# Performance work log

Hardware: AMD Instinct MI355X
Metric: run time of the kernel (lower is better)

The kernel has to match this reference:

```python
import jax, jax.numpy as jnp
import numpy as np

B, H, V, T = 2048, 512, 64, 128

def setup_inputs() -> dict:
    key = jax.random.key(0)
    ks = jax.random.split(key, 7)
    s = 1.0 / np.sqrt(H)
    return {
        "z": jax.random.normal(ks[0], (B, H), dtype=jnp.float32),
        "w_ih": jax.random.uniform(ks[1], (4 * H, H), jnp.float32, -s, s),
        "w_hh": jax.random.uniform(ks[2], (4 * H, H), jnp.float32, -s, s),
        "b_ih": jax.random.uniform(ks[3], (4 * H,), jnp.float32, -s, s),
        "b_hh": jax.random.uniform(ks[4], (4 * H,), jnp.float32, -s, s),
        "fc_w": jax.random.uniform(ks[5], (V, H), jnp.float32, -s, s),
        "fc_b": jax.random.uniform(ks[6], (V,), jnp.float32, -s, s),
    }

def reference(z, w_ih, w_hh, b_ih, b_hh, fc_w, fc_b):
    batch = z.shape[0]
    # Input z is identical at every timestep -> precompute its gate contribution once.
    x_gates = z @ w_ih.T + b_ih + b_hh  # [B, 4H]

    def step(carry, _):
        h, c = carry
        gates = x_gates + h @ w_hh.T  # [B, 4H]
        i, f, g, o = jnp.split(gates, 4, axis=-1)  # PyTorch LSTMCell gate order
        i = jax.nn.sigmoid(i)
        f = jax.nn.sigmoid(f)
        g = jnp.tanh(g)
        o = jax.nn.sigmoid(o)
        c = f * c + i * g
        h = o * jnp.tanh(c)
        return (h, c), h

    h0 = jnp.zeros((batch, w_hh.shape[1]), dtype=z.dtype)
    c0 = jnp.zeros_like(h0)
    _, hs = jax.lax.scan(step, (h0, c0), None, length=T)  # [T, B, H]
    x = jnp.transpose(hs, (1, 0, 2))  # [B, T, H]
    return jax.nn.relu(x @ fc_w.T + fc_b)  # [B, T, V]
```

## Files before the change

kernel.cpp:

```cpp
#include <hip/hip_runtime.h>
#include <hip/hip_bf16.h>
#include <cstdint>

#define B_   2048
#define H_   512
#define T_   128
#define V_   64
#define FOURH 2048

typedef __bf16 bf16x8 __attribute__((ext_vector_type(8)));
typedef float  floatx4 __attribute__((ext_vector_type(4)));
typedef int    intx4   __attribute__((ext_vector_type(4)));

__device__ __forceinline__ unsigned short f2bf(float f) {
    union { float f; uint32_t u; } v; v.f = f;
    uint32_t r = v.u + 0x7fff + ((v.u >> 16) & 1);
    return (unsigned short)(r >> 16);
}

__device__ __forceinline__ float rcp_(float x) {
    float r; asm("v_rcp_f32 %0, %1" : "=v"(r) : "v"(x)); return r;
}
__device__ __forceinline__ float sigmoidf_(float x) {
    return rcp_(1.0f + __expf(-x));
}
__device__ __forceinline__ float tanhf_(float x) {
    float e = __expf(fminf(-2.0f * x, 80.0f));
    return (1.0f - e) * rcp_(1.0f + e);
}

__device__ __forceinline__ void global_to_lds16(const unsigned short* g, unsigned short* l) {
    __builtin_amdgcn_global_load_lds(
        (const __attribute__((address_space(1))) unsigned int*)g,
        (__attribute__((address_space(3))) unsigned int*)l, 16, 0, 0);
}

__device__ __forceinline__ bf16x8 load16_sys(const unsigned short* p) {
    bf16x8 d;
    asm volatile("global_load_dwordx4 %0, %1, off sc0 sc1\n\t"
                 "s_waitcnt vmcnt(0)"
                 : "=v"(d) : "v"(p));
    return d;
}

__device__ __forceinline__ void flag_prefetch(const unsigned int* fp, intx4& f) {
    asm volatile("global_load_dwordx4 %0, %1, off sc0 sc1"
                 : "=v"(f) : "v"(fp) : "memory");
}
__device__ __forceinline__ bool flag_ok(const intx4& f, unsigned int tgt) {
    return (unsigned int)f[0] >= tgt && (unsigned int)f[1] >= tgt &&
           (unsigned int)f[2] >= tgt && (unsigned int)f[3] >= tgt;
}
__device__ __forceinline__ void wait4(const unsigned int* fp, unsigned int tgt) {
    for (;;) {
        intx4 f;
        asm volatile("global_load_dwordx4 %0, %1, off sc0 sc1\n\t"
                     "s_waitcnt vmcnt(0)" : "=v"(f) : "v"(fp) : "memory");
        if (flag_ok(f, tgt)) return;
        __builtin_amdgcn_s_sleep(1);
    }
}
__device__ __forceinline__ void flag_post(unsigned int* p, unsigned int v) {
    asm volatile("global_store_dword %0, %1, off sc0 sc1" :: "v"(p), "v"(v) : "memory");
}

__global__ void prep_kernel(const float* __restrict__ z,
                            const float* __restrict__ w_ih,
                            const float* __restrict__ w_hh,
                            const float* __restrict__ b_ih,
                            const float* __restrict__ b_hh,
                            const float* __restrict__ fc_w,
                            unsigned short* __restrict__ Bp_ih,
                            unsigned short* __restrict__ Bp_hh,
                            unsigned short* __restrict__ z_bf,
                            unsigned short* __restrict__ fcw_bf,
                            float* __restrict__ biasp,
                            unsigned int* __restrict__ cnt) {
    int i = blockIdx.x * blockDim.x + threadIdx.x;
    int col = i >> 9, k = i & 511;
    int jj = col >> 7, cc = col & 127;
    int gate = (cc >> 4) & 3;
    int hcl = ((cc >> 6) << 4) | (cc & 15);
    int p = gate * 512 + jj * 32 + hcl;
    Bp_hh[i] = f2bf(w_hh[p * 512 + k]);
    Bp_ih[i] = f2bf(w_ih[p * 512 + k]);
    z_bf[i]  = f2bf(z[i]);
    if (i < V_ * H_) fcw_bf[i] = f2bf(fc_w[i]);
    if (i < FOURH) {
        int j2 = i >> 7, c2 = i & 127;
        int g2 = (c2 >> 4) & 3;
        int h2 = ((c2 >> 6) << 4) | (c2 & 15);
        int p2 = g2 * 512 + j2 * 32 + h2;
        biasp[i] = b_ih[p2] + b_hh[p2];
    }
    if (i < 2048) cnt[i] = 0;
}

__device__ __forceinline__ void gemm_tile_r1(
        const unsigned short* __restrict__ Aglob,
        const unsigned short* __restrict__ Bglob,
        int arow0, int brow0,
        unsigned short* As, unsigned short* Bs,
        floatx4 acc[2][8], int w, int l) {
    const int lr = l >> 3;
    const int gl = (l & 7) ^ lr;
    const int ln = l & 15, lq = l >> 4, ls = l & 7;
    for (int kc = 0; kc < 8; ++kc) {
        const int kof = kc * 64 + gl * 8;
        #pragma unroll
        for (int q = 0; q < 4; ++q) {
            const int r0 = (w * 4 + q) * 8;
            global_to_lds16(Aglob + (size_t)(arow0 + r0 + lr) * 512 + kof, As + r0 * 64);
            global_to_lds16(Bglob + (size_t)(brow0 + r0 + lr) * 512 + kof, Bs + r0 * 64);
        }
        __syncthreads();
        #pragma unroll
        for (int kk = 0; kk < 2; ++kk) {
            bf16x8 a[2], b[8];
            #pragma unroll
            for (int mt = 0; mt < 2; ++mt) {
                const int m = 32 * w + 16 * mt + ln;
                const int g = kk * 4 + lq;
                a[mt] = *(const bf16x8*)(As + m * 64 + ((g ^ ls) * 8));
            }
            #pragma unroll
            for (int nt = 0; nt < 8; ++nt) {
                const int n = 16 * nt + ln;
                const int g = kk * 4 + lq;
                b[nt] = *(const bf16x8*)(Bs + n * 64 + ((g ^ ls) * 8));
            }
            #pragma unroll
            for (int mt = 0; mt < 2; ++mt)
                #pragma unroll
                for (int nt = 0; nt < 8; ++nt)
                    acc[mt][nt] = __builtin_amdgcn_mfma_f32_16x16x32_bf16(
                        a[mt], b[nt], acc[mt][nt], 0, 0, 0);
        }
        __syncthreads();
    }
}

__global__ void __launch_bounds__(256) xg_gemm_kernel(
        const unsigned short* __restrict__ z_bf,
        const unsigned short* __restrict__ Bp_ih,
        const float* __restrict__ biasp,
        float* __restrict__ xg) {
    __shared__ unsigned short As[128 * 64];
    __shared__ unsigned short Bs[128 * 64];
    const int bi = blockIdx.x, j = blockIdx.y;
    const int tid = threadIdx.x, w = tid >> 6, l = tid & 63;
    floatx4 acc[2][8];
    const floatx4 zf = {0.f, 0.f, 0.f, 0.f};
    for (int a1 = 0; a1 < 2; ++a1) for (int a2 = 0; a2 < 8; ++a2) acc[a1][a2] = zf;

    gemm_tile_r1(z_bf, Bp_ih, bi * 128, j * 128, As, Bs, acc, w, l);

    const int ln = l & 15, lq = l >> 4;
    #pragma unroll
    for (int mt = 0; mt < 2; ++mt)
        #pragma unroll
        for (int nt = 0; nt < 8; ++nt) {
            const int colp = j * 128 + nt * 16 + ln;
            const float bv = biasp[colp];
            #pragma unroll
            for (int r = 0; r < 4; ++r) {
                const int b = bi * 128 + 32 * w + 16 * mt + lq * 4 + r;
                xg[(size_t)b * FOURH + colp] = acc[mt][nt][r] + bv;
            }
        }
}

__device__ __forceinline__ void stage_issue2(const unsigned short* __restrict__ Aglob,
                                             int arow0, int kc, int w, int l,
                                             intx4& t0, intx4& t1) {
    const int lr = l >> 3;
    const int gl = (l & 7) ^ lr;
    const int kof = kc * 64 + gl * 8;
    const unsigned short* p0 = Aglob + (size_t)(arow0 + (w * 2 + 0) * 8 + lr) * 512 + kof;
    const unsigned short* p1 = Aglob + (size_t)(arow0 + (w * 2 + 1) * 8 + lr) * 512 + kof;
    asm volatile(
        "global_load_dwordx4 %0, %2, off sc0 sc1\n\t"
        "global_load_dwordx4 %1, %3, off sc0 sc1"
        : "=&v"(t0), "=&v"(t1)
        : "v"(p0), "v"(p1)
        : "memory");
}

template<int N>
__device__ __forceinline__ void commit4c(unsigned short* buf, int w, int l,
                                         const intx4* u) {
    if constexpr (N == 12) asm volatile("s_waitcnt vmcnt(12)" ::: "memory");
    else if constexpr (N == 8)  asm volatile("s_waitcnt vmcnt(8)"  ::: "memory");
    else if constexpr (N == 4)  asm volatile("s_waitcnt vmcnt(4)"  ::: "memory");
    else                        asm volatile("s_waitcnt vmcnt(0)"  ::: "memory");
    const int lr = l >> 3, sl = (l & 7) * 8;
    #pragma unroll
    for (int kcL = 0; kcL < 2; ++kcL)
        #pragma unroll
        for (int q = 0; q < 2; ++q)
            *(intx4*)(buf + kcL * 4096 + ((w * 2 + q) * 8 + lr) * 64 + sl) = u[kcL * 2 + q];
}

__global__ void __launch_bounds__(256, 1) lstm_persistent(
        const unsigned short* __restrict__ Bp_hh,
        const unsigned short* __restrict__ fcw_bf,
        const float* __restrict__ xg,
        const float* __restrict__ fc_b,
        unsigned short* __restrict__ h0b,
        unsigned short* __restrict__ h1b,
        unsigned int* __restrict__ cnt,
        float* __restrict__ out) {
    __shared__ unsigned short AsB0[4096 * 2];
    __shared__ unsigned short AsB1[4096 * 2];

    const int bx = blockIdx.x;
    const int gi = bx & 31;
    const int j  = bx >> 5;
    const int tid = threadIdx.x;
    const int w = tid >> 6, l = tid & 63;
    const int ln = l & 15, lq = l >> 4;
    const bool jlt4 = (j < 4);
    const int j16 = j * 16;
    const int v = 16 * w + ln;
    const float fcb_v = fc_b[v];
    const int arow0 = gi * 64;
    const int colbase = j * 256 + (w >> 1) * 128 + (w & 1) * 64;
    unsigned int* flagp = cnt + gi * 64;
    const floatx4 zf = {0.f, 0.f, 0.f, 0.f};

    bf16x8 bq[16][4];
    {
        const unsigned short* bbase =
            Bp_hh + ((size_t)(colbase + ln)) * 512 + lq * 8;
        #pragma unroll
        for (int s = 0; s < 16; ++s)
            #pragma unroll
            for (int nt = 0; nt < 4; ++nt)
                bq[s][nt] = *(const bf16x8*)(bbase + (size_t)nt * 16 * 512 + s * 32);
    }

    floatx4 xga[4][4];
    #pragma unroll
    for (int mt = 0; mt < 4; ++mt)
        #pragma unroll
        for (int nt = 0; nt < 4; ++nt)
            #pragma unroll
            for (int r = 0; r < 4; ++r) {
                const int b = arow0 + 16 * mt + lq * 4 + r;
                xga[mt][nt][r] = xg[(size_t)b * FOURH + colbase + 16 * nt + ln];
            }

    for (int d = 0; d < gi; ++d) __builtin_amdgcn_s_sleep(15);

    unsigned short* hlds = AsB0;

    float cst[4][4];
    #pragma unroll
    for (int mt = 0; mt < 4; ++mt)
        #pragma unroll
        for (int r = 0; r < 4; ++r) {
            float iv = sigmoidf_(xga[mt][0][r]);
            float gv = tanhf_  (xga[mt][2][r]);
            float ov = sigmoidf_(xga[mt][3][r]);
            float cv = iv * gv;
            cst[mt][r] = cv;
            hlds[(16 * mt + lq * 4 + r) * 64 + (16 * w + ln)] = f2bf(ov * tanhf_(cv));
        }
    __syncthreads();
    for (int c = tid; c < 512; c += 256) {
        const int row = c >> 3, seg = c & 7;
        intx4 d = *(const intx4*)(hlds + row * 64 + seg * 8);
        const unsigned short* p = h0b + (size_t)(arow0 + row) * 512 + j * 64 + seg * 8;
        asm volatile("global_store_dwordx4 %0, %1, off sc0 sc1" :: "v"(p), "v"(d) : "memory");
    }
    asm volatile("s_waitcnt vmcnt(0)" ::: "memory");
    __syncthreads();
    if (tid == 0) flag_post(flagp + j, 1u);
    intx4 fpreA, fpreB;
    flag_prefetch(flagp,     fpreA);
    flag_prefetch(flagp + 4, fpreB);

    unsigned short* hb[2] = {h0b, h1b};
    #pragma unroll 1
    for (int t = 1; t < T_; ++t) {
        const unsigned int tg = (unsigned int)t;

        asm volatile("s_waitcnt vmcnt(0)" ::: "memory");
        __builtin_amdgcn_sched_barrier(0);
        if (!(flag_ok(fpreA, tg) && flag_ok(fpreB, tg))) {
            wait4(flagp, tg);
            wait4(flagp + 4, tg);
        }

        const unsigned short* hprev = hb[(t - 1) & 1];
        unsigned short* hnext = hb[t & 1];

        floatx4 acc[4][4];
        #pragma unroll
        for (int a1 = 0; a1 < 4; ++a1)
            #pragma unroll
            for (int a2 = 0; a2 < 4; ++a2) acc[a1][a2] = zf;
        floatx4 pacc = zf;

        intx4 u[16];
        #pragma unroll
        for (int g = 0; g < 4; ++g) {
            stage_issue2(hprev, arow0, 2 * g,     w, l, u[4 * g + 0], u[4 * g + 1]);
            stage_issue2(hprev, arow0, 2 * g + 1, w, l, u[4 * g + 2], u[4 * g + 3]);
        }
        commit4c<12>(AsB0, w, l, &u[0]);
        __syncthreads();

        #pragma unroll
        for (int g = 0; g < 4; ++g) {
            const unsigned short* buf = (g & 1) ? AsB1 : AsB0;
            #pragma unroll
            for (int ss = 0; ss < 4; ++ss) {
                const int s = g * 4 + ss;
                const int ga = (ss & 1) * 4 + lq;
                const unsigned short* Ac = buf + (ss >> 1) * 4096;
                bf16x8 af[4];
                #pragma unroll
                for (int mt = 0; mt < 4; ++mt) {
                    const int m = 16 * mt + ln;
                    af[mt] = *(const bf16x8*)(Ac + m * 64 + ((ga ^ (ln & 7)) * 8));
                }
                #pragma unroll
                for (int mt = 0; mt < 4; ++mt)
                    #pragma unroll
                    for (int nt = 0; nt < 4; ++nt)
                        acc[mt][nt] = __builtin_amdgcn_mfma_f32_16x16x32_bf16(
                            af[mt], bq[s][nt], acc[mt][nt], 0, 0, 0);
                if (jlt4) {
                    bf16x8 ap = *(const bf16x8*)(Ac + (j16 + ln) * 64 + ((ga ^ (ln & 7)) * 8));
                    bf16x8 bp = *(const bf16x8*)(fcw_bf + (size_t)v * 512 + s * 32 + lq * 8);
                    pacc = __builtin_amdgcn_mfma_f32_16x16x32_bf16(ap, bp, pacc, 0, 0, 0);
                }
            }
            if (g == 0) { commit4c<8>(AsB1, w, l, &u[4]);  __syncthreads(); }
            else if (g == 1) { commit4c<4>(AsB0, w, l, &u[8]);  __syncthreads(); }
            else if (g == 2) { commit4c<0>(AsB1, w, l, &u[12]); __syncthreads(); }
        }

        #pragma unroll
        for (int mt = 0; mt < 4; ++mt)
            #pragma unroll
            for (int r = 0; r < 4; ++r) {
                float iv = sigmoidf_(acc[mt][0][r] + xga[mt][0][r]);
                float fv = sigmoidf_(acc[mt][1][r] + xga[mt][1][r]);
                float gv = tanhf_  (acc[mt][2][r] + xga[mt][2][r]);
                float ov = sigmoidf_(acc[mt][3][r] + xga[mt][3][r]);
                float cn = fv * cst[mt][r] + iv * gv;
                cst[mt][r] = cn;
                hlds[(16 * mt + lq * 4 + r) * 64 + (16 * w + ln)] = f2bf(ov * tanhf_(cn));
            }
        __syncthreads();
        for (int c = tid; c < 512; c += 256) {
            const int row = c >> 3, seg = c & 7;
            intx4 d = *(const intx4*)(hlds + row * 64 + seg * 8);
            const unsigned short* p = hnext + (size_t)(arow0 + row) * 512 + j * 64 + seg * 8;
            asm volatile("global_store_dwordx4 %0, %1, off sc0 sc1" :: "v"(p), "v"(d) : "memory");
        }
        asm volatile("s_waitcnt vmcnt(0)" ::: "memory");
        __syncthreads();
        if (tid == 0) flag_post(flagp + j, tg + 1u);

        if (jlt4) {
            #pragma unroll
            for (int r = 0; r < 4; ++r) {
                const int b = arow0 + j16 + lq * 4 + r;
                out[(size_t)b * (T_ * V_) + (t - 1) * V_ + v] = fmaxf(pacc[r] + fcb_v, 0.0f);
            }
        }
        flag_prefetch(flagp,     fpreA);
        flag_prefetch(flagp + 4, fpreB);
    }

    if (jlt4) {
        wait4(flagp,     T_);
        wait4(flagp + 4, T_);
        const unsigned short* hlast = hb[(T_ - 1) & 1];
        floatx4 pa = zf;
        const int ar = arow0 + j16 + ln;
        #pragma unroll
        for (int kc = 0; kc < 16; ++kc) {
            const int k = kc * 32 + lq * 8;
            bf16x8 a = load16_sys(hlast + (size_t)ar * 512 + k);
            bf16x8 b = *(const bf16x8*)(fcw_bf + (size_t)v * 512 + k);
            pa = __builtin_amdgcn_mfma_f32_16x16x32_bf16(a, b, pa, 0, 0, 0);
        }
        #pragma unroll
        for (int r = 0; r < 4; ++r) {
            const int b = arow0 + j16 + lq * 4 + r;
            out[(size_t)b * (T_ * V_) + (T_ - 1) * V_ + v] = fmaxf(pa[r] + fcb_v, 0.0f);
        }
    }
}

extern "C" void kernel_launch(void* const* d_in, const int* in_sizes, int n_in,
                              void* d_out, int out_size, void* d_ws, size_t ws_size,
                              hipStream_t stream) {
    const float* z    = (const float*)d_in[0];
    const float* w_ih = (const float*)d_in[1];
    const float* w_hh = (const float*)d_in[2];
    const float* b_ih = (const float*)d_in[3];
    const float* b_hh = (const float*)d_in[4];
    const float* fc_w = (const float*)d_in[5];
    const float* fc_b = (const float*)d_in[6];
    float* out = (float*)d_out;

    char* ws = (char*)d_ws;
    size_t o = 0;
    auto take = [&](size_t bytes) { char* p = ws + o; o += (bytes + 255) & ~(size_t)255; return p; };
    unsigned short* Bp_hh  = (unsigned short*)take((size_t)FOURH * H_ * 2);
    unsigned short* Bp_ih  = (unsigned short*)take((size_t)FOURH * H_ * 2);
    unsigned short* z_bf   = (unsigned short*)take((size_t)B_ * H_ * 2);
    unsigned short* fcw_bf = (unsigned short*)take((size_t)V_ * H_ * 2);
    float*          biasp  = (float*)take((size_t)FOURH * 4);
    unsigned short* hbuf0  = (unsigned short*)take((size_t)B_ * H_ * 2);
    unsigned short* hbuf1  = (unsigned short*)take((size_t)B_ * H_ * 2);
    unsigned int*   cnt    = (unsigned int*)take(32 * 256);
    float*          xg     = (float*)take((size_t)B_ * FOURH * 4);

    prep_kernel<<<(B_ * H_) / 256, 256, 0, stream>>>(z, w_ih, w_hh, b_ih, b_hh, fc_w,
                                                     Bp_ih, Bp_hh, z_bf, fcw_bf, biasp, cnt);
    xg_gemm_kernel<<<dim3(16, 16), 256, 0, stream>>>(z_bf, Bp_ih, biasp, xg);
    lstm_persistent<<<256, 256, 0, stream>>>(Bp_hh, fcw_bf, xg, fc_b,
                                             hbuf0, hbuf1, cnt, out);
}
```

Before: 1.483 ms.

## Split batch tile into two half-phases to overlap h exchange with compute

```diff
diff --git a/kernel.cpp b/kernel.cpp
--- a/kernel.cpp
+++ b/kernel.cpp
@@ -170,35 +170,123 @@
         }
 }
 
-__device__ __forceinline__ void stage_issue2(const unsigned short* __restrict__ Aglob,
-                                             int arow0, int kc, int w, int l,
-                                             intx4& t0, intx4& t1) {
-    const int lr = l >> 3;
-    const int gl = (l & 7) ^ lr;
-    const int kof = kc * 64 + gl * 8;
-    const unsigned short* p0 = Aglob + (size_t)(arow0 + (w * 2 + 0) * 8 + lr) * 512 + kof;
-    const unsigned short* p1 = Aglob + (size_t)(arow0 + (w * 2 + 1) * 8 + lr) * 512 + kof;
-    asm volatile(
-        "global_load_dwordx4 %0, %2, off sc0 sc1\n\t"
-        "global_load_dwordx4 %1, %3, off sc0 sc1"
-        : "=&v"(t0), "=&v"(t1)
-        : "v"(p0), "v"(p1)
-        : "memory");
-}
-
-template<int N>
-__device__ __forceinline__ void commit4c(unsigned short* buf, int w, int l,
-                                         const intx4* u) {
-    if constexpr (N == 12) asm volatile("s_waitcnt vmcnt(12)" ::: "memory");
-    else if constexpr (N == 8)  asm volatile("s_waitcnt vmcnt(8)"  ::: "memory");
-    else if constexpr (N == 4)  asm volatile("s_waitcnt vmcnt(4)"  ::: "memory");
-    else                        asm volatile("s_waitcnt vmcnt(0)"  ::: "memory");
-    const int lr = l >> 3, sl = (l & 7) * 8;
-    #pragma unroll
-    for (int kcL = 0; kcL < 2; ++kcL)
-        #pragma unroll
-        for (int q = 0; q < 2; ++q)
-            *(intx4*)(buf + kcL * 4096 + ((w * 2 + q) * 8 + lr) * 64 + sl) = u[kcL * 2 + q];
+template<int HF>
+__device__ __forceinline__ void phase_body(
+        int t, bool last,
+        int arow0, int j, int tid, int w, int l, int ln, int lq,
+        bool my_half, int j16, int v, float fcb_v,
+        unsigned short* hb0, unsigned short* hb1,
+        unsigned int* flagp,
+        unsigned short* Xlds, unsigned short* hlds,
+        const unsigned short* __restrict__ fcw_bf,
+        const bf16x8 (&bq)[16][4],
+        floatx4 (&acc)[2][4], float (&cst)[2][4], const floatx4 (&xga)[2][4],
+        floatx4& pacc, float* __restrict__ out,
+        intx4 (&u)[8], intx4& fp0, intx4& fp1)
+{
+    const unsigned int V = (unsigned int)t + (unsigned int)HF;
+    const int foff = 8 * (1 - HF);
+    unsigned short* hbt[2] = {hb0, hb1};
+    const floatx4 zf = {0.f, 0.f, 0.f, 0.f};
+
+    asm volatile("s_waitcnt vmcnt(0)" ::: "memory");
+    __builtin_amdgcn_sched_barrier(0);
+
+    if (tid == 0) flag_post(flagp + foff + j, V);
+    {
+        const int lr = l >> 3, sl = (l & 7) * 8;
+        #pragma unroll
+        for (int kc = 0; kc < 8; ++kc)
+            *(intx4*)(Xlds + kc * 2048 + (w * 8 + lr) * 64 + sl) = u[kc];
+    }
+    __syncthreads();
+
+    if (!last) {
+        flag_prefetch(flagp + foff,     fp0);
+        flag_prefetch(flagp + foff + 4, fp1);
+    }
+    if (my_half) pacc = zf;
+    #pragma unroll
+    for (int s = 0; s < 16; ++s) {
+        const int ga = (s & 1) * 4 + lq;
+        const unsigned short* Ac = Xlds + (s >> 1) * 2048;
+        bf16x8 af[2];
+        #pragma unroll
+        for (int mt = 0; mt < 2; ++mt)
+            af[mt] = *(const bf16x8*)(Ac + (16 * mt + ln) * 64 + ((ga ^ (ln & 7)) * 8));
+        #pragma unroll
+        for (int mt = 0; mt < 2; ++mt)
+            #pragma unroll
+            for (int nt = 0; nt < 4; ++nt)
+                acc[mt][nt] = __builtin_amdgcn_mfma_f32_16x16x32_bf16(
+                    af[mt], bq[s][nt], acc[mt][nt], 0, 0, 0);
+        if (my_half) {
+            bf16x8 ap = *(const bf16x8*)(Ac + ((j16 & 31) + ln) * 64 + ((ga ^ (ln & 7)) * 8));
+            bf16x8 bp = *(const bf16x8*)(fcw_bf + (size_t)v * 512 + s * 32 + lq * 8);
+            pacc = __builtin_amdgcn_mfma_f32_16x16x32_bf16(ap, bp, pacc, 0, 0, 0);
+        }
+    }
+
+    if (!last) {
+        asm volatile("s_waitcnt vmcnt(0)" ::: "memory");
+        __builtin_amdgcn_sched_barrier(0);
+        if (!(flag_ok(fp0, V) && flag_ok(fp1, V))) {
+            wait4(flagp + foff,     V);
+            wait4(flagp + foff + 4, V);
+        }
+        if (my_half) {
+            #pragma unroll
+            for (int r = 0; r < 4; ++r) {
+                const int b = arow0 + j16 + lq * 4 + r;
+                out[(size_t)b * (T_ * V_) + (t - 1) * V_ + v] = fmaxf(pacc[r] + fcb_v, 0.0f);
+            }
+        }
+        {
+            const unsigned short* src = hbt[(t - 1 + HF) & 1]
+                                      + (size_t)(arow0 + (1 - HF) * 32) * 512;
+            const int lr = l >> 3;
+            const int gl = (l & 7) ^ lr;
+            #pragma unroll
+            for (int kc = 0; kc < 8; ++kc) {
+                const unsigned short* p = src + (size_t)(w * 8 + lr) * 512 + kc * 64 + gl * 8;
+                asm volatile("global_load_dwordx4 %0, %1, off sc0 sc1"
+                             : "=&v"(u[kc]) : "v"(p) : "memory");
+            }
+        }
+    } else {
+        if (my_half) {
+            #pragma unroll
+            for (int r = 0; r < 4; ++r) {
+                const int b = arow0 + j16 + lq * 4 + r;
+                out[(size_t)b * (T_ * V_) + (t - 1) * V_ + v] = fmaxf(pacc[r] + fcb_v, 0.0f);
+            }
+        }
+    }
+
+    #pragma unroll
+    for (int mt = 0; mt < 2; ++mt)
+        #pragma unroll
+        for (int r = 0; r < 4; ++r) {
+            float iv = sigmoidf_(acc[mt][0][r] + xga[mt][0][r]);
+            float fv = sigmoidf_(acc[mt][1][r] + xga[mt][1][r]);
+            float gv = tanhf_  (acc[mt][2][r] + xga[mt][2][r]);
+            float ov = sigmoidf_(acc[mt][3][r] + xga[mt][3][r]);
+            float cn = fv * cst[mt][r] + iv * gv;
+            cst[mt][r] = cn;
+            hlds[(16 * mt + lq * 4 + r) * 64 + (16 * w + ln)] = f2bf(ov * tanhf_(cn));
+        }
+    #pragma unroll
+    for (int mt = 0; mt < 2; ++mt)
+        #pragma unroll
+        for (int nt = 0; nt < 4; ++nt) acc[mt][nt] = zf;
+    __syncthreads();
+    {
+        const int row = tid >> 3, seg = tid & 7;
+        intx4 d = *(const intx4*)(hlds + row * 64 + seg * 8);
+        const unsigned short* p = hbt[t & 1]
+                                + (size_t)(arow0 + HF * 32 + row) * 512 + j * 64 + seg * 8;
+        asm volatile("global_store_dwordx4 %0, %1, off sc0 sc1" :: "v"(p), "v"(d) : "memory");
+    }
 }
 
 __global__ void __launch_bounds__(256, 1) lstm_persistent(
@@ -210,8 +298,9 @@
         unsigned short* __restrict__ h1b,
         unsigned int* __restrict__ cnt,
         float* __restrict__ out) {
-    __shared__ unsigned short AsB0[4096 * 2];
-    __shared__ unsigned short AsB1[4096 * 2];
+    __shared__ unsigned short Alds[8 * 2048];
+    __shared__ unsigned short Blds[8 * 2048];
+    __shared__ unsigned short hlds[2048];
 
     const int bx = blockIdx.x;
     const int gi = bx & 31;
@@ -227,6 +316,8 @@
     const int colbase = j * 256 + (w >> 1) * 128 + (w & 1) * 64;
     unsigned int* flagp = cnt + gi * 64;
     const floatx4 zf = {0.f, 0.f, 0.f, 0.f};
+    const bool myA = jlt4 && (j < 2);
+    const bool myB = jlt4 && (j >= 2);
 
     bf16x8 bq[16][4];
     {
@@ -239,147 +330,105 @@
                 bq[s][nt] = *(const bf16x8*)(bbase + (size_t)nt * 16 * 512 + s * 32);
     }
 
-    floatx4 xga[4][4];
-    #pragma unroll
-    for (int mt = 0; mt < 4; ++mt)
+    floatx4 xgaA[2][4], xgaB[2][4];
+    #pragma unroll
+    for (int mt = 0; mt < 2; ++mt)
         #pragma unroll
         for (int nt = 0; nt < 4; ++nt)
             #pragma unroll
             for (int r = 0; r < 4; ++r) {
-                const int b = arow0 + 16 * mt + lq * 4 + r;
-                xga[mt][nt][r] = xg[(size_t)b * FOURH + colbase + 16 * nt + ln];
+                const int ba = arow0 + 16 * mt + lq * 4 + r;
+                const int bb = arow0 + 32 + 16 * mt + lq * 4 + r;
+                xgaA[mt][nt][r] = xg[(size_t)ba * FOURH + colbase + 16 * nt + ln];
+                xgaB[mt][nt][r] = xg[(size_t)bb * FOURH + colbase + 16 * nt + ln];
             }
 
     for (int d = 0; d < gi; ++d) __builtin_amdgcn_s_sleep(15);
 
-    unsigned short* hlds = AsB0;
-
-    float cst[4][4];
-    #pragma unroll
-    for (int mt = 0; mt < 4; ++mt)
+    float cstA[2][4], cstB[2][4];
+    floatx4 accA[2][4], accB[2][4];
+    #pragma unroll
+    for (int mt = 0; mt < 2; ++mt)
+        #pragma unroll
+        for (int nt = 0; nt < 4; ++nt) { accA[mt][nt] = zf; accB[mt][nt] = zf; }
+
+    #pragma unroll
+    for (int mt = 0; mt < 2; ++mt)
         #pragma unroll
         for (int r = 0; r < 4; ++r) {
-            float iv = sigmoidf_(xga[mt][0][r]);
-            float gv = tanhf_  (xga[mt][2][r]);
-            float ov = sigmoidf_(xga[mt][3][r]);
+            float iv = sigmoidf_(xgaA[mt][0][r]);
+            float gv = tanhf_  (xgaA[mt][2][r]);
+            float ov = sigmoidf_(xgaA[mt][3][r]);
             float cv = iv * gv;
-            cst[mt][r] = cv;
+            cstA[mt][r] = cv;
             hlds[(16 * mt + lq * 4 + r) * 64 + (16 * w + ln)] = f2bf(ov * tanhf_(cv));
         }
     __syncthreads();
-    for (int c = tid; c < 512; c += 256) {
-        const int row = c >> 3, seg = c & 7;
+    {
+        const int row = tid >> 3, seg = tid & 7;
         intx4 d = *(const intx4*)(hlds + row * 64 + seg * 8);
         const unsigned short* p = h0b + (size_t)(arow0 + row) * 512 + j * 64 + seg * 8;
         asm volatile("global_store_dwordx4 %0, %1, off sc0 sc1" :: "v"(p), "v"(d) : "memory");
     }
+    __syncthreads();
+    #pragma unroll
+    for (int mt = 0; mt < 2; ++mt)
+        #pragma unroll
+        for (int r = 0; r < 4; ++r) {
+            float iv = sigmoidf_(xgaB[mt][0][r]);
+            float gv = tanhf_  (xgaB[mt][2][r]);
+            float ov = sigmoidf_(xgaB[mt][3][r]);
+            float cv = iv * gv;
+            cstB[mt][r] = cv;
+            hlds[(16 * mt + lq * 4 + r) * 64 + (16 * w + ln)] = f2bf(ov * tanhf_(cv));
+        }
+    __syncthreads();
+    {
+        const int row = tid >> 3, seg = tid & 7;
+        intx4 d = *(const intx4*)(hlds + row * 64 + seg * 8);
+        const unsigned short* p = h0b + (size_t)(arow0 + 32 + row) * 512 + j * 64 + seg * 8;
+        asm volatile("global_store_dwordx4 %0, %1, off sc0 sc1" :: "v"(p), "v"(d) : "memory");
+    }
     asm volatile("s_waitcnt vmcnt(0)" ::: "memory");
     __syncthreads();
-    if (tid == 0) flag_post(flagp + j, 1u);
-    intx4 fpreA, fpreB;
-    flag_prefetch(flagp,     fpreA);
-    flag_prefetch(flagp + 4, fpreB);
-
-    unsigned short* hb[2] = {h0b, h1b};
+    if (tid == 0) { flag_post(flagp + j, 1u); flag_post(flagp + 8 + j, 1u); }
+
+    wait4(flagp,     1u);
+    wait4(flagp + 4, 1u);
+    intx4 u[8];
+    {
+        const unsigned short* src = h0b + (size_t)arow0 * 512;
+        const int lr = l >> 3;
+        const int gl = (l & 7) ^ lr;
+        #pragma unroll
+        for (int kc = 0; kc < 8; ++kc) {
+            const unsigned short* p = src + (size_t)(w * 8 + lr) * 512 + kc * 64 + gl * 8;
+            asm volatile("global_load_dwordx4 %0, %1, off sc0 sc1"
+                         : "=&v"(u[kc]) : "v"(p) : "memory");
+        }
+    }
+
+    floatx4 pacc = zf;
+    intx4 fp0, fp1;
     #pragma unroll 1
     for (int t = 1; t < T_; ++t) {
-        const unsigned int tg = (unsigned int)t;
-
-        asm volatile("s_waitcnt vmcnt(0)" ::: "memory");
-        __builtin_amdgcn_sched_barrier(0);
-        if (!(flag_ok(fpreA, tg) && flag_ok(fpreB, tg))) {
-            wait4(flagp, tg);
-            wait4(flagp + 4, tg);
-        }
-
-        const unsigned short* hprev = hb[(t - 1) & 1];
-        unsigned short* hnext = hb[t & 1];
-
-        floatx4 acc[4][4];
-        #pragma unroll
-        for (int a1 = 0; a1 < 4; ++a1)
-            #pragma unroll
-            for (int a2 = 0; a2 < 4; ++a2) acc[a1][a2] = zf;
-        floatx4 pacc = zf;
-
-        intx4 u[16];
-        #pragma unroll
-        for (int g = 0; g < 4; ++g) {
-            stage_issue2(hprev, arow0, 2 * g,     w, l, u[4 * g + 0], u[4 * g + 1]);
-            stage_issue2(hprev, arow0, 2 * g + 1, w, l, u[4 * g + 2], u[4 * g + 3]);
-        }
-        commit4c<12>(AsB0, w, l, &u[0]);
-        __syncthreads();
-
-        #pragma unroll
-        for (int g = 0; g < 4; ++g) {
-            const unsigned short* buf = (g & 1) ? AsB1 : AsB0;
-            #pragma unroll
-            for (int ss = 0; ss < 4; ++ss) {
-                const int s = g * 4 + ss;
-                const int ga = (ss & 1) * 4 + lq;
-                const unsigned short* Ac = buf + (ss >> 1) * 4096;
-                bf16x8 af[4];
-                #pragma unroll
-                for (int mt = 0; mt < 4; ++mt) {
-                    const int m = 16 * mt + ln;
-                    af[mt] = *(const bf16x8*)(Ac + m * 64 + ((ga ^ (ln & 7)) * 8));
-                }
-                #pragma unroll
-                for (int mt = 0; mt < 4; ++mt)
-                    #pragma unroll
-                    for (int nt = 0; nt < 4; ++nt)
-                        acc[mt][nt] = __builtin_amdgcn_mfma_f32_16x16x32_bf16(
-                            af[mt], bq[s][nt], acc[mt][nt], 0, 0, 0);
-                if (jlt4) {
-                    bf16x8 ap = *(const bf16x8*)(Ac + (j16 + ln) * 64 + ((ga ^ (ln & 7)) * 8));
-                    bf16x8 bp = *(const bf16x8*)(fcw_bf + (size_t)v * 512 + s * 32 + lq * 8);
-                    pacc = __builtin_amdgcn_mfma_f32_16x16x32_bf16(ap, bp, pacc, 0, 0, 0);
-                }
-            }
-            if (g == 0) { commit4c<8>(AsB1, w, l, &u[4]);  __syncthreads(); }
-            else if (g == 1) { commit4c<4>(AsB0, w, l, &u[8]);  __syncthreads(); }
-            else if (g == 2) { commit4c<0>(AsB1, w, l, &u[12]); __syncthreads(); }
-        }
-
-        #pragma unroll
-        for (int mt = 0; mt < 4; ++mt)
-            #pragma unroll
-            for (int r = 0; r < 4; ++r) {
-                float iv = sigmoidf_(acc[mt][0][r] + xga[mt][0][r]);
-                float fv = sigmoidf_(acc[mt][1][r] + xga[mt][1][r]);
-                float gv = tanhf_  (acc[mt][2][r] + xga[mt][2][r]);
-                float ov = sigmoidf_(acc[mt][3][r] + xga[mt][3][r]);
-                float cn = fv * cst[mt][r] + iv * gv;
-                cst[mt][r] = cn;
-                hlds[(16 * mt + lq * 4 + r) * 64 + (16 * w + ln)] = f2bf(ov * tanhf_(cn));
-            }
-        __syncthreads();
-        for (int c = tid; c < 512; c += 256) {
-            const int row = c >> 3, seg = c & 7;
-            intx4 d = *(const intx4*)(hlds + row * 64 + seg * 8);
-            const unsigned short* p = hnext + (size_t)(arow0 + row) * 512 + j * 64 + seg * 8;
-            asm volatile("global_store_dwordx4 %0, %1, off sc0 sc1" :: "v"(p), "v"(d) : "memory");
-        }
-        asm volatile("s_waitcnt vmcnt(0)" ::: "memory");
-        __syncthreads();
-        if (tid == 0) flag_post(flagp + j, tg + 1u);
-
-        if (jlt4) {
-            #pragma unroll
-            for (int r = 0; r < 4; ++r) {
-                const int b = arow0 + j16 + lq * 4 + r;
-                out[(size_t)b * (T_ * V_) + (t - 1) * V_ + v] = fmaxf(pacc[r] + fcb_v, 0.0f);
-            }
-        }
-        flag_prefetch(flagp,     fpreA);
-        flag_prefetch(flagp + 4, fpreB);
-    }
+        phase_body<0>(t, false, arow0, j, tid, w, l, ln, lq, myA, j16, v, fcb_v,
+                      h0b, h1b, flagp, Alds, hlds, fcw_bf, bq,
+                      accA, cstA, xgaA, pacc, out, u, fp0, fp1);
+        phase_body<1>(t, t == T_ - 1, arow0, j, tid, w, l, ln, lq, myB, j16, v, fcb_v,
+                      h0b, h1b, flagp, Blds, hlds, fcw_bf, bq,
+                      accB, cstB, xgaB, pacc, out, u, fp0, fp1);
+    }
+
+    asm volatile("s_waitcnt vmcnt(0)" ::: "memory");
+    __syncthreads();
+    if (tid == 0) flag_post(flagp + 8 + j, (unsigned int)T_);
 
     if (jlt4) {
-        wait4(flagp,     T_);
-        wait4(flagp + 4, T_);
-        const unsigned short* hlast = hb[(T_ - 1) & 1];
+        const int hf = (j >= 2);
+        wait4(flagp + 8 * hf,     (unsigned int)T_);
+        wait4(flagp + 8 * hf + 4, (unsigned int)T_);
+        const unsigned short* hlast = h1b;
         floatx4 pa = zf;
         const int ar = arow0 + j16 + ln;
         #pragma unroll
```

Result: faster. 1.417 ms (-4.4%).

## Split batch group into four 16-row slices with per-slice flags for pipelined recurrence

Applied to the files above, without the earlier changes.

```diff
diff --git a/kernel.cpp b/kernel.cpp
--- a/kernel.cpp
+++ b/kernel.cpp
@@ -170,35 +170,113 @@
         }
 }
 
-__device__ __forceinline__ void stage_issue2(const unsigned short* __restrict__ Aglob,
-                                             int arow0, int kc, int w, int l,
-                                             intx4& t0, intx4& t1) {
-    const int lr = l >> 3;
-    const int gl = (l & 7) ^ lr;
-    const int kof = kc * 64 + gl * 8;
-    const unsigned short* p0 = Aglob + (size_t)(arow0 + (w * 2 + 0) * 8 + lr) * 512 + kof;
-    const unsigned short* p1 = Aglob + (size_t)(arow0 + (w * 2 + 1) * 8 + lr) * 512 + kof;
-    asm volatile(
-        "global_load_dwordx4 %0, %2, off sc0 sc1\n\t"
-        "global_load_dwordx4 %1, %3, off sc0 sc1"
-        : "=&v"(t0), "=&v"(t1)
-        : "v"(p0), "v"(p1)
-        : "memory");
-}
-
-template<int N>
-__device__ __forceinline__ void commit4c(unsigned short* buf, int w, int l,
-                                         const intx4* u) {
-    if constexpr (N == 12) asm volatile("s_waitcnt vmcnt(12)" ::: "memory");
-    else if constexpr (N == 8)  asm volatile("s_waitcnt vmcnt(8)"  ::: "memory");
-    else if constexpr (N == 4)  asm volatile("s_waitcnt vmcnt(4)"  ::: "memory");
-    else                        asm volatile("s_waitcnt vmcnt(0)"  ::: "memory");
-    const int lr = l >> 3, sl = (l & 7) * 8;
-    #pragma unroll
-    for (int kcL = 0; kcL < 2; ++kcL)
-        #pragma unroll
-        for (int q = 0; q < 2; ++q)
-            *(intx4*)(buf + kcL * 4096 + ((w * 2 + q) * 8 + lr) * 64 + sl) = u[kcL * 2 + q];
+__device__ __forceinline__ void issue_slice(const unsigned short* __restrict__ src,
+                                            int w, int l, intx4 (&u)[4]) {
+    const int r = w * 4 + (l >> 4);
+    const int il = l & 15, slot = il & 7;
+    #pragma unroll
+    for (int i = 0; i < 4; ++i) {
+        const int kc = i * 2 + (il >> 3);
+        const unsigned short* p = src + (size_t)r * 512 + kc * 64 + ((slot ^ (r & 7)) * 8);
+        asm volatile("global_load_dwordx4 %0, %1, off sc0 sc1"
+                     : "=&v"(u[i]) : "v"(p) : "memory");
+    }
+}
+
+template<int X>
+__device__ __forceinline__ void phase4(
+        int t,
+        int arow0, int j, int tid, int w, int l, int ln, int lq,
+        unsigned short* h0b, unsigned short* h1b,
+        unsigned int* flagp,
+        unsigned short* Xlds, unsigned short* hlds,
+        const unsigned short* __restrict__ fcw_bf,
+        const bf16x8 (&bq)[16][4],
+        float (&cst)[4], const floatx4 (&xga)[4],
+        float fcb_v, int v, float* __restrict__ out,
+        intx4 (&u)[4], intx4& fpA, intx4& fpB)
+{
+    constexpr int Z   = (X + 2) & 3;
+    constexpr int DZ  = (X + 2) >> 2;
+    constexpr int Zn  = (X + 3) & 3;
+    constexpr int DZn = (X + 3) >> 2;
+    const bool mine = (j == X);
+    const floatx4 zf = {0.f, 0.f, 0.f, 0.f};
+
+    {
+        const int r = w * 4 + lq;
+        const int il = l & 15, slot = il & 7;
+        #pragma unroll
+        for (int i = 0; i < 4; ++i) {
+            const int kc = i * 2 + (il >> 3);
+            *(intx4*)(Xlds + kc * 1024 + r * 64 + slot * 8) = u[i];
+        }
+    }
+    __syncthreads();
+
+    floatx4 acc[4];
+    #pragma unroll
+    for (int nt = 0; nt < 4; ++nt) acc[nt] = zf;
+    floatx4 pacc = zf;
+    #pragma unroll
+    for (int s = 0; s < 16; ++s) {
+        const int ga = (s & 1) * 4 + lq;
+        const unsigned short* Ac = Xlds + (s >> 1) * 1024;
+        bf16x8 af = *(const bf16x8*)(Ac + ln * 64 + ((ga ^ (ln & 7)) * 8));
+        #pragma unroll
+        for (int nt = 0; nt < 4; ++nt)
+            acc[nt] = __builtin_amdgcn_mfma_f32_16x16x32_bf16(
+                af, bq[s][nt], acc[nt], 0, 0, 0);
+        if (mine) {
+            bf16x8 bp = *(const bf16x8*)(fcw_bf + (size_t)v * 512 + s * 32 + lq * 8);
+            pacc = __builtin_amdgcn_mfma_f32_16x16x32_bf16(af, bp, pacc, 0, 0, 0);
+        }
+    }
+
+    asm volatile("s_waitcnt vmcnt(0)" ::: "memory");
+    __builtin_amdgcn_sched_barrier(0);
+    if (t + DZ < T_) {
+        const unsigned int tz = (unsigned int)(t + DZ);
+        if (!(flag_ok(fpA, tz) && flag_ok(fpB, tz))) {
+            wait4(flagp + Z * 8,     tz);
+            wait4(flagp + Z * 8 + 4, tz);
+        }
+        const unsigned short* src = (((t + DZ - 1) & 1) ? h1b : h0b)
+                                  + (size_t)(arow0 + Z * 16) * 512;
+        issue_slice(src, w, l, u);
+    }
+    if (mine) {
+        #pragma unroll
+        for (int r = 0; r < 4; ++r) {
+            const int b = arow0 + j * 16 + lq * 4 + r;
+            out[(size_t)b * (T_ * V_) + (t - 1) * V_ + v] = fmaxf(pacc[r] + fcb_v, 0.0f);
+        }
+    }
+    if (t + DZn < T_) {
+        flag_prefetch(flagp + Zn * 8,     fpA);
+        flag_prefetch(flagp + Zn * 8 + 4, fpB);
+    }
+
+    #pragma unroll
+    for (int r = 0; r < 4; ++r) {
+        float iv = sigmoidf_(acc[0][r] + xga[0][r]);
+        float fv = sigmoidf_(acc[1][r] + xga[1][r]);
+        float gv = tanhf_  (acc[2][r] + xga[2][r]);
+        float ov = sigmoidf_(acc[3][r] + xga[3][r]);
+        float cn = fv * cst[r] + iv * gv;
+        cst[r] = cn;
+        hlds[(lq * 4 + r) * 64 + (16 * w + ln)] = f2bf(ov * tanhf_(cn));
+    }
+    __syncthreads();
+    if (tid < 128) {
+        const int row = tid >> 3, seg = tid & 7;
+        intx4 d = *(const intx4*)(hlds + row * 64 + seg * 8);
+        unsigned short* hn = (t & 1) ? h1b : h0b;
+        const unsigned short* p = hn + (size_t)(arow0 + X * 16 + row) * 512 + j * 64 + seg * 8;
+        asm volatile("global_store_dwordx4 %0, %1, off sc0 sc1" :: "v"(p), "v"(d) : "memory");
+    }
+    __syncthreads();
+    if (tid == 0) flag_post(flagp + X * 8 + j, (unsigned int)(t + 1));
 }
 
 __global__ void __launch_bounds__(256, 1) lstm_persistent(
@@ -210,8 +288,9 @@
         unsigned short* __restrict__ h1b,
         unsigned int* __restrict__ cnt,
         float* __restrict__ out) {
-    __shared__ unsigned short AsB0[4096 * 2];
-    __shared__ unsigned short AsB1[4096 * 2];
+    __shared__ unsigned short lds0[8 * 1024];
+    __shared__ unsigned short lds1[8 * 1024];
+    __shared__ unsigned short hlds[1024];
 
     const int bx = blockIdx.x;
     const int gi = bx & 31;
@@ -220,7 +299,6 @@
     const int w = tid >> 6, l = tid & 63;
     const int ln = l & 15, lq = l >> 4;
     const bool jlt4 = (j < 4);
-    const int j16 = j * 16;
     const int v = 16 * w + ln;
     const float fcb_v = fc_b[v];
     const int arow0 = gi * 64;
@@ -239,149 +317,94 @@
                 bq[s][nt] = *(const bf16x8*)(bbase + (size_t)nt * 16 * 512 + s * 32);
     }
 
-    floatx4 xga[4][4];
-    #pragma unroll
-    for (int mt = 0; mt < 4; ++mt)
-        #pragma unroll
-        for (int nt = 0; nt < 4; ++nt)
-            #pragma unroll
-            for (int r = 0; r < 4; ++r) {
-                const int b = arow0 + 16 * mt + lq * 4 + r;
-                xga[mt][nt][r] = xg[(size_t)b * FOURH + colbase + 16 * nt + ln];
-            }
+    floatx4 xga0[4], xga1[4], xga2[4], xga3[4];
+    #pragma unroll
+    for (int nt = 0; nt < 4; ++nt)
+        #pragma unroll
+        for (int r = 0; r < 4; ++r) {
+            const int rb = lq * 4 + r;
+            xga0[nt][r] = xg[(size_t)(arow0 +      rb) * FOURH + colbase + 16 * nt + ln];
+            xga1[nt][r] = xg[(size_t)(arow0 + 16 + rb) * FOURH + colbase + 16 * nt + ln];
+            xga2[nt][r] = xg[(size_t)(arow0 + 32 + rb) * FOURH + colbase + 16 * nt + ln];
+            xga3[nt][r] = xg[(size_t)(arow0 + 48 + rb) * FOURH + colbase + 16 * nt + ln];
+        }
 
     for (int d = 0; d < gi; ++d) __builtin_amdgcn_s_sleep(15);
 
-    unsigned short* hlds = AsB0;
-
-    float cst[4][4];
-    #pragma unroll
-    for (int mt = 0; mt < 4; ++mt)
-        #pragma unroll
-        for (int r = 0; r < 4; ++r) {
-            float iv = sigmoidf_(xga[mt][0][r]);
-            float gv = tanhf_  (xga[mt][2][r]);
-            float ov = sigmoidf_(xga[mt][3][r]);
-            float cv = iv * gv;
-            cst[mt][r] = cv;
-            hlds[(16 * mt + lq * 4 + r) * 64 + (16 * w + ln)] = f2bf(ov * tanhf_(cv));
-        }
-    __syncthreads();
-    for (int c = tid; c < 512; c += 256) {
-        const int row = c >> 3, seg = c & 7;
-        intx4 d = *(const intx4*)(hlds + row * 64 + seg * 8);
-        const unsigned short* p = h0b + (size_t)(arow0 + row) * 512 + j * 64 + seg * 8;
-        asm volatile("global_store_dwordx4 %0, %1, off sc0 sc1" :: "v"(p), "v"(d) : "memory");
-    }
+    float cst0[4], cst1[4], cst2[4], cst3[4];
+#define PRO_SLICE(S, XGA, CST)                                                \
+    {                                                                         \
+        _Pragma("unroll")                                                     \
+        for (int r = 0; r < 4; ++r) {                                         \
+            float iv = sigmoidf_(XGA[0][r]);                                  \
+            float gv = tanhf_  (XGA[2][r]);                                   \
+            float ov = sigmoidf_(XGA[3][r]);                                  \
+            float cv = iv * gv;                                               \
+            CST[r] = cv;                                                      \
+            hlds[(lq * 4 + r) * 64 + (16 * w + ln)] = f2bf(ov * tanhf_(cv));  \
+        }                                                                     \
+        __syncthreads();                                                      \
+        if (tid < 128) {                                                      \
+            const int row = tid >> 3, seg = tid & 7;                          \
+            intx4 d = *(const intx4*)(hlds + row * 64 + seg * 8);             \
+            const unsigned short* p = h0b                                     \
+                + (size_t)(arow0 + S * 16 + row) * 512 + j * 64 + seg * 8;    \
+            asm volatile("global_store_dwordx4 %0, %1, off sc0 sc1"           \
+                         :: "v"(p), "v"(d) : "memory");                       \
+        }                                                                     \
+        __syncthreads();                                                      \
+    }
+    PRO_SLICE(0, xga0, cst0)
+    PRO_SLICE(1, xga1, cst1)
+    PRO_SLICE(2, xga2, cst2)
+    PRO_SLICE(3, xga3, cst3)
+#undef PRO_SLICE
     asm volatile("s_waitcnt vmcnt(0)" ::: "memory");
     __syncthreads();
-    if (tid == 0) flag_post(flagp + j, 1u);
-    intx4 fpreA, fpreB;
-    flag_prefetch(flagp,     fpreA);
-    flag_prefetch(flagp + 4, fpreB);
-
-    unsigned short* hb[2] = {h0b, h1b};
+    if (tid == 0) {
+        flag_post(flagp +  0 + j, 1u);
+        flag_post(flagp +  8 + j, 1u);
+        flag_post(flagp + 16 + j, 1u);
+        flag_post(flagp + 24 + j, 1u);
+    }
+
+    wait4(flagp +  0, 1u); wait4(flagp +  4, 1u);
+    wait4(flagp +  8, 1u); wait4(flagp + 12, 1u);
+    intx4 uE[4], uO[4], fpA, fpB;
+    issue_slice(h0b + (size_t)(arow0)      * 512, w, l, uE);
+    issue_slice(h0b + (size_t)(arow0 + 16) * 512, w, l, uO);
+    flag_prefetch(flagp + 16, fpA);
+    flag_prefetch(flagp + 20, fpB);
+    asm volatile("s_waitcnt vmcnt(0)" ::: "memory");
+    __builtin_amdgcn_sched_barrier(0);
+
     #pragma unroll 1
     for (int t = 1; t < T_; ++t) {
-        const unsigned int tg = (unsigned int)t;
-
-        asm volatile("s_waitcnt vmcnt(0)" ::: "memory");
-        __builtin_amdgcn_sched_barrier(0);
-        if (!(flag_ok(fpreA, tg) && flag_ok(fpreB, tg))) {
-            wait4(flagp, tg);
-            wait4(flagp + 4, tg);
-        }
-
-        const unsigned short* hprev = hb[(t - 1) & 1];
-        unsigned short* hnext = hb[t & 1];
-
-        floatx4 acc[4][4];
-        #pragma unroll
-        for (int a1 = 0; a1 < 4; ++a1)
-            #pragma unroll
-            for (int a2 = 0; a2 < 4; ++a2) acc[a1][a2] = zf;
-        floatx4 pacc = zf;
-
-        intx4 u[16];
-        #pragma unroll
-        for (int g = 0; g < 4; ++g) {
-            stage_issue2(hprev, arow0, 2 * g,     w, l, u[4 * g + 0], u[4 * g + 1]);
-            stage_issue2(hprev, arow0, 2 * g + 1, w, l, u[4 * g + 2], u[4 * g + 3]);
-        }
-        commit4c<12>(AsB0, w, l, &u[0]);
-        __syncthreads();
-
-        #pragma unroll
-        for (int g = 0; g < 4; ++g) {
-            const unsigned short* buf = (g & 1) ? AsB1 : AsB0;
-            #pragma unroll
-            for (int ss = 0; ss < 4; ++ss) {
-                const int s = g * 4 + ss;
-                const int ga = (ss & 1) * 4 + lq;
-                const unsigned short* Ac = buf + (ss >> 1) * 4096;
-                bf16x8 af[4];
-                #pragma unroll
-                for (int mt = 0; mt < 4; ++mt) {
-                    const int m = 16 * mt + ln;
-                    af[mt] = *(const bf16x8*)(Ac + m * 64 + ((ga ^ (ln & 7)) * 8));
-                }
-                #pragma unroll
-                for (int mt = 0; mt < 4; ++mt)
-                    #pragma unroll
-                    for (int nt = 0; nt < 4; ++nt)
-                        acc[mt][nt] = __builtin_amdgcn_mfma_f32_16x16x32_bf16(
-                            af[mt], bq[s][nt], acc[mt][nt], 0, 0, 0);
-                if (jlt4) {
-                    bf16x8 ap = *(const bf16x8*)(Ac + (j16 + ln) * 64 + ((ga ^ (ln & 7)) * 8));
-                    bf16x8 bp = *(const bf16x8*)(fcw_bf + (size_t)v * 512 + s * 32 + lq * 8);
-                    pacc = __builtin_amdgcn_mfma_f32_16x16x32_bf16(ap, bp, pacc, 0, 0, 0);
-                }
-            }
-            if (g == 0) { commit4c<8>(AsB1, w, l, &u[4]);  __syncthreads(); }
-            else if (g == 1) { commit4c<4>(AsB0, w, l, &u[8]);  __syncthreads(); }
-            else if (g == 2) { commit4c<0>(AsB1, w, l, &u[12]); __syncthreads(); }
-        }
-
-        #pragma unroll
-        for (int mt = 0; mt < 4; ++mt)
-            #pragma unroll
-            for (int r = 0; r < 4; ++r) {
-                float iv = sigmoidf_(acc[mt][0][r] + xga[mt][0][r]);
-                float fv = sigmoidf_(acc[mt][1][r] + xga[mt][1][r]);
-                float gv = tanhf_  (acc[mt][2][r] + xga[mt][2][r]);
-                float ov = sigmoidf_(acc[mt][3][r] + xga[mt][3][r]);
-                float cn = fv * cst[mt][r] + iv * gv;
-                cst[mt][r] = cn;
-                hlds[(16 * mt + lq * 4 + r) * 64 + (16 * w + ln)] = f2bf(ov * tanhf_(cn));
-            }
-        __syncthreads();
-        for (int c = tid; c < 512; c += 256) {
-            const int row = c >> 3, seg = c & 7;
-            intx4 d = *(const intx4*)(hlds + row * 64 + seg * 8);
-            const unsigned short* p = hnext + (size_t)(arow0 + row) * 512 + j * 64 + seg * 8;
-            asm volatile("global_store_dwordx4 %0, %1, off sc0 sc1" :: "v"(p), "v"(d) : "memory");
-        }
-        asm volatile("s_waitcnt vmcnt(0)" ::: "memory");
-        __syncthreads();
-        if (tid == 0) flag_post(flagp + j, tg + 1u);
-
-        if (jlt4) {
-            #pragma unroll
-            for (int r = 0; r < 4; ++r) {
-                const int b = arow0 + j16 + lq * 4 + r;
-                out[(size_t)b * (T_ * V_) + (t - 1) * V_ + v] = fmaxf(pacc[r] + fcb_v, 0.0f);
-            }
-        }
-        flag_prefetch(flagp,     fpreA);
-        flag_prefetch(flagp + 4, fpreB);
+        phase4<0>(t, arow0, j, tid, w, l, ln, lq, h0b, h1b, flagp, lds0, hlds,
+                  fcw_bf, bq, cst0, xga0, fcb_v, v, out, uE, fpA, fpB);
+        phase4<1>(t, arow0, j, tid, w, l, ln, lq, h0b, h1b, flagp, lds1, hlds,
+                  fcw_bf, bq, cst1, xga1, fcb_v, v, out, uO, fpA, fpB);
+        phase4<2>(t, arow0, j, tid, w, l, ln, lq, h0b, h1b, flagp, lds0, hlds,
+                  fcw_bf, bq, cst2, xga2, fcb_v, v, out, uE, fpA, fpB);
+        phase4<3>(t, arow0, j, tid, w, l, ln, lq, h0b, h1b, flagp, lds1, hlds,
+                  fcw_bf, bq, cst3, xga3, fcb_v, v, out, uO, fpA, fpB);
+    }
+
+    asm volatile("s_waitcnt vmcnt(0)" ::: "memory");
+    __syncthreads();
+    if (tid == 0) {
+        flag_post(flagp +  0 + j, (unsigned int)T_);
+        flag_post(flagp +  8 + j, (unsigned int)T_);
+        flag_post(flagp + 16 + j, (unsigned int)T_);
+        flag_post(flagp + 24 + j, (unsigned int)T_);
     }
 
     if (jlt4) {
-        wait4(flagp,     T_);
-        wait4(flagp + 4, T_);
-        const unsigned short* hlast = hb[(T_ - 1) & 1];
+        wait4(flagp + j * 8,     (unsigned int)T_);
+        wait4(flagp + j * 8 + 4, (unsigned int)T_);
+        const unsigned short* hlast = h1b;
         floatx4 pa = zf;
-        const int ar = arow0 + j16 + ln;
+        const int ar = arow0 + j * 16 + ln;
         #pragma unroll
         for (int kc = 0; kc < 16; ++kc) {
             const int k = kc * 32 + lq * 8;
@@ -391,7 +414,7 @@
         }
         #pragma unroll
         for (int r = 0; r < 4; ++r) {
-            const int b = arow0 + j16 + lq * 4 + r;
+            const int b = arow0 + j * 16 + lq * 4 + r;
             out[(size_t)b * (T_ * V_) + (T_ - 1) * V_ + v] = fmaxf(pa[r] + fcb_v, 0.0f);
         }
     }
```

Result: faster. 1.394 ms (-6.0%).
